# Optimization experiments

Measured on AMD Instinct MI355X. Metric: run time of the kernel, lower is better.

Reference implementation:

```python
import jax, jax.numpy as jnp
import numpy as np

N = 20000      # nodes
E = 320000     # edges
F = 32         # node_feat_dim
H = 128        # hidden_dim
HEADS = 4
DH = 128       # out_channels per head (PyG TransformerConv semantics)
L = 2          # number of GNNBlocks actually built


def _ln(x, s, b, eps=1e-5):
    m = x.mean(-1, keepdims=True)
    v = ((x - m) ** 2).mean(-1, keepdims=True)
    return (x - m) / jnp.sqrt(v + eps) * s + b


def setup_inputs() -> dict:
    key = jax.random.key(0)
    ks = jax.random.split(key, 16)
    nrm = lambda k, sh, sc=0.05: jax.random.normal(k, sh, dtype=jnp.float32) * sc
    inp = {}
    inp['x'] = jax.random.normal(ks[0], (N, F), dtype=jnp.float32)
    inp['edge_index'] = jax.random.randint(ks[1], (2, E), 0, N)
    inp['Win'] = nrm(ks[2], (F, H))
    inp['b_in'] = jnp.zeros((H,), jnp.float32)
    inp['ln1_s'] = jnp.ones((L, H), jnp.float32)
    inp['ln1_b'] = jnp.zeros((L, H), jnp.float32)
    inp['Wq'] = nrm(ks[3], (L, H, HEADS * DH))
    inp['bq'] = jnp.zeros((L, HEADS * DH), jnp.float32)
    inp['Wk'] = nrm(ks[4], (L, H, HEADS * DH))
    inp['bk'] = jnp.zeros((L, HEADS * DH), jnp.float32)
    inp['Wv'] = nrm(ks[5], (L, H, HEADS * DH))
    inp['bv'] = jnp.zeros((L, HEADS * DH), jnp.float32)
    inp['Wskip'] = nrm(ks[6], (L, H, H))
    inp['bskip'] = jnp.zeros((L, H), jnp.float32)
    inp['Wbeta'] = nrm(ks[7], (L, 3 * H, 1))
    inp['ln2_s'] = jnp.ones((L, H), jnp.float32)
    inp['ln2_b'] = jnp.zeros((L, H), jnp.float32)
    inp['W1'] = nrm(ks[8], (L, H, 4 * H))
    inp['b1'] = jnp.zeros((L, 4 * H), jnp.float32)
    inp['W2'] = nrm(ks[9], (L, 4 * H, H))
    inp['b2'] = jnp.zeros((L, H), jnp.float32)
    inp['g1'] = jnp.ones((L,), jnp.float32)
    inp['g2'] = jnp.ones((L,), jnp.float32)
    inp['lno_s'] = jnp.ones((H,), jnp.float32)
    inp['lno_b'] = jnp.zeros((H,), jnp.float32)
    return inp


def reference(x, edge_index, Win, b_in, ln1_s, ln1_b, Wq, bq, Wk, bk, Wv, bv,
              Wskip, bskip, Wbeta, ln2_s, ln2_b, W1, b1, W2, b2, g1, g2,
              lno_s, lno_b):
    src, dst = edge_index[0], edge_index[1]  # messages flow src -> dst
    n = x.shape[0]
    scale = 1.0 / np.sqrt(DH).astype(np.float32)
    h = x @ Win + b_in  # [N,H]
    for l in range(L):
        # --- pre-norm TransformerConv (heads=4, concat=False, beta=True) ---
        hn = _ln(h, ln1_s[l], ln1_b[l])
        q = (hn @ Wq[l] + bq[l]).reshape(n, HEADS, DH)
        k = (hn @ Wk[l] + bk[l]).reshape(n, HEADS, DH)
        v = (hn @ Wv[l] + bv[l]).reshape(n, HEADS, DH)
        # per-edge attention logits [E, HEADS]
        alpha = jnp.einsum('ehd,ehd->eh', q[dst], k[src]) * scale
        # segment softmax over incoming edges of each target node
        amax = jax.ops.segment_max(alpha, dst, num_segments=n)  # [N,HEADS]
        num = jnp.exp(alpha - amax[dst])
        den = jax.ops.segment_sum(num, dst, num_segments=n)      # [N,HEADS]
        a = num / den[dst]                                       # [E,HEADS]
        # scatter-aggregate weighted values, then mean over heads (concat=False)
        agg = jax.ops.segment_sum(a[:, :, None] * v[src], dst, num_segments=n)
        out = agg.mean(axis=1)                                   # [N,H]
        # root skip + beta gate
        xr = hn @ Wskip[l] + bskip[l]
        beta = jax.nn.sigmoid(
            jnp.concatenate([out, xr, out - xr], axis=-1) @ Wbeta[l])  # [N,1]
        attn = beta * xr + (1.0 - beta) * out
        h = h + g1[l] * attn
        # --- pre-norm FFN ---
        hn2 = _ln(h, ln2_s[l], ln2_b[l])
        ffn = jax.nn.gelu(hn2 @ W1[l] + b1[l], approximate=False) @ W2[l] + b2[l]
        h = h + g2[l] * ffn
    return _ln(h, lno_s, lno_b)
```

## Files before the change

kernel.cpp:

```cpp
#include <hip/hip_runtime.h>
#include <hip/hip_bf16.h>
#include <math.h>

#define NN 20000
#define NE 320000

typedef unsigned short ushort_t;
typedef unsigned short ushortx8 __attribute__((ext_vector_type(8)));
typedef short s16x8 __attribute__((ext_vector_type(8)));
typedef float f32x4 __attribute__((ext_vector_type(4)));
typedef float f32x2 __attribute__((ext_vector_type(2)));

__device__ __forceinline__ float us2f(unsigned short u){
  return __uint_as_float(((unsigned)u) << 16);
}
__device__ __forceinline__ unsigned short f2us(float f){
  unsigned u = __float_as_uint(f);
  unsigned r = (u + 0x7fffu + ((u >> 16) & 1u)) >> 16;
  return (unsigned short)r;
}
__device__ __forceinline__ void e4m3x8_to_f32(uint2 d, float* out){
  f32x2 a = __builtin_amdgcn_cvt_pk_f32_fp8(d.x, false);
  f32x2 b = __builtin_amdgcn_cvt_pk_f32_fp8(d.x, true);
  f32x2 c = __builtin_amdgcn_cvt_pk_f32_fp8(d.y, false);
  f32x2 e = __builtin_amdgcn_cvt_pk_f32_fp8(d.y, true);
  out[0] = a.x; out[1] = a.y; out[2] = b.x; out[3] = b.y;
  out[4] = c.x; out[5] = c.y; out[6] = e.x; out[7] = e.y;
}
__device__ __forceinline__ uint2 f32x8_to_e4m3(const float* f){
  unsigned lo = __builtin_amdgcn_cvt_pk_fp8_f32(f[0], f[1], 0u, false);
  lo = __builtin_amdgcn_cvt_pk_fp8_f32(f[2], f[3], lo, true);
  unsigned hi = __builtin_amdgcn_cvt_pk_fp8_f32(f[4], f[5], 0u, false);
  hi = __builtin_amdgcn_cvt_pk_fp8_f32(f[6], f[7], hi, true);
  return make_uint2(lo, hi);
}

__global__ void k_hist(const int* __restrict__ ei, int* __restrict__ deg){
  int e = blockIdx.x * 256 + threadIdx.x;
  if (e < NE) atomicAdd(&deg[ei[NE + e]], 1);
}

__global__ __launch_bounds__(1024) void k_scan(const int* __restrict__ deg,
                                               int* __restrict__ rowst,
                                               int* __restrict__ cur){
  __shared__ int s[1024];
  __shared__ int carry_s;
  int tid = threadIdx.x;
  if (tid == 0) carry_s = 0;
  __syncthreads();
  for (int base = 0; base < NN; base += 1024){
    int v = (base + tid < NN) ? deg[base + tid] : 0;
    s[tid] = v; __syncthreads();
    for (int off = 1; off < 1024; off <<= 1){
      int t = (tid >= off) ? s[tid - off] : 0;
      __syncthreads();
      s[tid] += t;
      __syncthreads();
    }
    int carry = carry_s;
    int excl = carry + s[tid] - v;
    if (base + tid < NN){ rowst[base + tid] = excl; cur[base + tid] = excl; }
    __syncthreads();
    if (tid == 0) carry_s = carry + s[1023];
    __syncthreads();
  }
  if (tid == 0) rowst[NN] = carry_s;
}

__global__ void k_scatter(const int* __restrict__ ei, int* __restrict__ cur,
                          int* __restrict__ srcs){
  int e = blockIdx.x * 256 + threadIdx.x;
  if (e < NE){
    int s = ei[e];
    int d = ei[NE + e];
    int p = atomicAdd(&cur[d], 1);
    srcs[p] = s;
  }
}

__global__ void k_wt(const float* __restrict__ Wq, const float* __restrict__ Wk,
                     const float* __restrict__ Wv, const float* __restrict__ Wsk,
                     const float* __restrict__ W1, const float* __restrict__ W2,
                     const float* __restrict__ bq, const float* __restrict__ bk,
                     const float* __restrict__ bv, const float* __restrict__ bsk,
                     ushort_t* __restrict__ out, float* __restrict__ bcat,
                     int* __restrict__ deg){
  int f = blockIdx.x * 256 + threadIdx.x;
  if (f < 688128){
    float val;
    if (f < 425984){
      int l = f / 212992, idx = f % 212992;
      int n = idx / 128, kk = idx % 128;
      if (n < 512)       val = Wq[(size_t)l * 65536 + kk * 512 + n];
      else if (n < 1024) val = Wk[(size_t)l * 65536 + kk * 512 + (n - 512)];
      else if (n < 1536) val = Wv[(size_t)l * 65536 + kk * 512 + (n - 1024)];
      else               val = Wsk[(size_t)l * 16384 + kk * 128 + (n - 1536)];
    } else if (f < 557056){
      int idx = f - 425984;
      int l = idx / 65536, r = idx % 65536;
      int n = r / 128, kk = r % 128;
      val = W1[(size_t)l * 65536 + kk * 512 + n];
    } else {
      int idx = f - 557056;
      int l = idx / 65536, r = idx % 65536;
      int n = r / 512, kk = r % 512;
      val = W2[(size_t)l * 65536 + kk * 128 + n];
    }
    out[f] = f2us(val);
  } else if (f < 691456){
    int i = f - 688128;
    int l = i / 1664, c = i % 1664;
    float v;
    if (c < 512)       v = bq[l * 512 + c];
    else if (c < 1024) v = bk[l * 512 + c - 512];
    else if (c < 1536) v = bv[l * 512 + c - 1024];
    else               v = bsk[l * 128 + c - 1536];
    bcat[i] = v;
  } else if (f < 711456){
    deg[f - 691456] = 0;
  }
}

__global__ __launch_bounds__(128) void k_inproj(const float* __restrict__ x,
                                                const float* __restrict__ Win,
                                                const float* __restrict__ bin,
                                                float* __restrict__ h){
  __shared__ float sW[32 * 128];
  __shared__ float sx[4][32];
  int tid = threadIdx.x;
  for (int i = 0; i < 32; i++) sW[i * 128 + tid] = Win[i * 128 + tid];
  int r0 = blockIdx.x * 4;
  {
    int r = tid >> 5, kk = tid & 31;
    int gr = r0 + r;
    sx[r][kk] = (gr < NN) ? x[gr * 32 + kk] : 0.f;
  }
  __syncthreads();
  float bias = bin[tid];
  for (int r = 0; r < 4; r++){
    int gr = r0 + r;
    if (gr >= NN) break;
    float acc = bias;
    #pragma unroll
    for (int k2 = 0; k2 < 32; k2++) acc += sx[r][k2] * sW[k2 * 128 + tid];
    h[(size_t)gr * 128 + tid] = acc;
  }
}

template<int OUTBF16>
__global__ void k_ln(const float* __restrict__ in, const float* __restrict__ sc,
                     const float* __restrict__ bi, void* __restrict__ outp, int rows){
  int row = blockIdx.x * 4 + (threadIdx.x >> 6);
  int lane = threadIdx.x & 63;
  if (row >= rows) return;
  const float* p = in + (size_t)row * 128 + lane * 2;
  float x0 = p[0], x1 = p[1];
  float sum = x0 + x1;
  for (int m = 1; m < 64; m <<= 1) sum += __shfl_xor(sum, m);
  float mean = sum * (1.f / 128.f);
  float d0 = x0 - mean, d1 = x1 - mean;
  float vs = d0 * d0 + d1 * d1;
  for (int m = 1; m < 64; m <<= 1) vs += __shfl_xor(vs, m);
  float rstd = rsqrtf(vs * (1.f / 128.f) + 1e-5f);
  int d = lane * 2;
  float o0 = d0 * rstd * sc[d] + bi[d];
  float o1 = d1 * rstd * sc[d + 1] + bi[d + 1];
  if (OUTBF16){
    ushort_t* o = (ushort_t*)outp + (size_t)row * 128 + d;
    o[0] = f2us(o0); o[1] = f2us(o1);
  } else {
    float* o = (float*)outp + (size_t)row * 128 + d;
    o[0] = o0; o[1] = o1;
  }
}

template<int MODE>
__global__ __launch_bounds__(256) void k_mm(const ushort_t* __restrict__ A, int M, int K,
                                            const ushort_t* __restrict__ Bt,
                                            const float* __restrict__ bias,
                                            void* __restrict__ Cp, int ldc,
                                            const float* __restrict__ gptr,
                                            ushort_t* __restrict__ qout,
                                            unsigned char* __restrict__ kvout,
                                            ushort_t* __restrict__ xrout){
  __shared__ ushort_t smem[2 * 128 * 72];
  ushort_t* As = smem;
  ushort_t* Bs = smem + 128 * 72;
  int tid = threadIdx.x;
  int m0 = blockIdx.x * 128, n0 = blockIdx.y * 128;
  int lane = tid & 63, w = tid >> 6;
  int wm = (w >> 1) * 64, wn = (w & 1) * 64;
  int fr = lane & 15, fq = lane >> 4;
  f32x4 acc[4][4];
  #pragma unroll
  for (int i = 0; i < 4; i++)
    #pragma unroll
    for (int j = 0; j < 4; j++) acc[i][j] = (f32x4){0.f, 0.f, 0.f, 0.f};

  for (int k0 = 0; k0 < K; k0 += 64){
    __syncthreads();
    #pragma unroll
    for (int it = 0; it < 4; it++){
      int idx = it * 256 + tid;
      int row = idx >> 3, ks = (idx & 7) * 8;
      int gr = m0 + row; if (gr >= M) gr = M - 1;
      *(ushortx8*)&As[row * 72 + ks] = *(const ushortx8*)(A + (size_t)gr * K + k0 + ks);
      *(ushortx8*)&Bs[row * 72 + ks] = *(const ushortx8*)(Bt + (size_t)(n0 + row) * K + k0 + ks);
    }
    __syncthreads();
    #pragma unroll
    for (int ks = 0; ks < 64; ks += 32){
      s16x8 a[4], b[4];
      #pragma unroll
      for (int i = 0; i < 4; i++)
        a[i] = *(const s16x8*)&As[(wm + i * 16 + fr) * 72 + ks + fq * 8];
      #pragma unroll
      for (int j = 0; j < 4; j++)
        b[j] = *(const s16x8*)&Bs[(wn + j * 16 + fr) * 72 + ks + fq * 8];
      #pragma unroll
      for (int i = 0; i < 4; i++)
        #pragma unroll
        for (int j = 0; j < 4; j++)
          acc[i][j] = __builtin_amdgcn_mfma_f32_16x16x32_bf16(a[i], b[j], acc[i][j], 0, 0, 0);
    }
  }

  if (MODE == 2){
    float g = *gptr;
    #pragma unroll
    for (int i = 0; i < 4; i++){
      int grb = m0 + wm + i * 16 + fq * 4;
      #pragma unroll
      for (int r = 0; r < 4; r++){
        int gr = grb + r;
        if (gr >= M) continue;
        #pragma unroll
        for (int j = 0; j < 4; j++){
          int gc = n0 + wn + j * 16 + fr;
          float c = acc[i][j][r] + bias[gc];
          ((float*)Cp)[(size_t)gr * ldc + gc] += g * c;
        }
      }
    }
    return;
  }

  __syncthreads();
  ushort_t* Cs = smem;
  #pragma unroll
  for (int i = 0; i < 4; i++){
    int rowb = wm + i * 16 + fq * 4;
    #pragma unroll
    for (int j = 0; j < 4; j++){
      int col = wn + j * 16 + fr;
      float bv = bias[n0 + col];
      #pragma unroll
      for (int r = 0; r < 4; r++){
        float c = acc[i][j][r] + bv;
        if (MODE == 1) c = 0.5f * c * (1.f + erff(c * 0.70710678118654752f));
        Cs[(rowb + r) * 136 + col] = f2us(c);
      }
    }
  }
  __syncthreads();
  #pragma unroll
  for (int it = 0; it < 8; it++){
    int idx = it * 256 + tid;
    int row = idx >> 4, seg = idx & 15;
    int gr = m0 + row;
    if (gr >= M) continue;
    ushortx8 cv = *(const ushortx8*)&Cs[row * 136 + seg * 8];
    int gc = n0 + seg * 8;
    if (MODE == 1){
      *(ushortx8*)((ushort_t*)Cp + (size_t)gr * ldc + gc) = cv;
    } else {
      if (n0 < 512){
        *(ushortx8*)(qout + (size_t)gr * 512 + gc) = cv;
      } else if (n0 < 1536){
        float fv[8];
        #pragma unroll
        for (int t = 0; t < 8; t++) fv[t] = us2f(cv[t]);
        *(uint2*)(kvout + (size_t)gr * 1024 + (gc - 512)) = f32x8_to_e4m3(fv);
      } else {
        *(ushortx8*)(xrout + (size_t)gr * 128 + (gc - 1536)) = cv;
      }
    }
  }
}

__global__ void k_alpha(const ushort_t* __restrict__ q, const unsigned char* __restrict__ kv8,
                        const int* __restrict__ rowst, const int* __restrict__ srcs,
                        float* __restrict__ alw){
  int n = blockIdx.x * 4 + (threadIdx.x >> 6);
  int lane = threadIdx.x & 63;
  if (n >= NN) return;
  int s0 = rowst[n], s1 = rowst[n + 1];
  if (s0 == s1) return;
  ushortx8 qv = *((const ushortx8*)(q + (size_t)n * 512) + lane);
  float qf[8];
  #pragma unroll
  for (int t = 0; t < 8; t++) qf[t] = us2f(qv[t]);
  const float scale = 0.08838834764831845f;
  int head = lane >> 4;
  for (int c0 = s0; c0 < s1; c0 += 64){
    int rem = s1 - c0; if (rem > 64) rem = 64;
    int se = (lane < rem) ? srcs[c0 + lane] : 0;
    int j = 0;
    for (; j + 4 <= rem; j += 4){
      int sv[4];
      #pragma unroll
      for (int u = 0; u < 4; u++) sv[u] = __shfl(se, j + u);
      uint2 kd[4];
      #pragma unroll
      for (int u = 0; u < 4; u++)
        kd[u] = *((const uint2*)(kv8 + (size_t)sv[u] * 1024) + lane);
      float p[4] = {0.f, 0.f, 0.f, 0.f};
      #pragma unroll
      for (int u = 0; u < 4; u++){
        float kf[8];
        e4m3x8_to_f32(kd[u], kf);
        #pragma unroll
        for (int t = 0; t < 8; t++) p[u] += qf[t] * kf[t];
      }
      #pragma unroll
      for (int u = 0; u < 4; u++){
        p[u] += __shfl_xor(p[u], 1); p[u] += __shfl_xor(p[u], 2);
        p[u] += __shfl_xor(p[u], 4); p[u] += __shfl_xor(p[u], 8);
      }
      if ((lane & 15) == 0){
        #pragma unroll
        for (int u = 0; u < 4; u++) alw[(size_t)(c0 + j + u) * 4 + head] = __expf(p[u] * scale);
      }
    }
    for (; j < rem; j++){
      int sv0 = __shfl(se, j);
      uint2 kd = *((const uint2*)(kv8 + (size_t)sv0 * 1024) + lane);
      float kf[8];
      e4m3x8_to_f32(kd, kf);
      float p0 = 0.f;
      #pragma unroll
      for (int t = 0; t < 8; t++) p0 += qf[t] * kf[t];
      p0 += __shfl_xor(p0, 1); p0 += __shfl_xor(p0, 2);
      p0 += __shfl_xor(p0, 4); p0 += __shfl_xor(p0, 8);
      if ((lane & 15) == 0) alw[(size_t)(c0 + j) * 4 + head] = __expf(p0 * scale);
    }
  }
}

__global__ void k_node(const float* __restrict__ alw, const unsigned char* __restrict__ kv8,
                       const int* __restrict__ rowst, const int* __restrict__ srcs,
                       const ushort_t* __restrict__ xr, const float* __restrict__ Wb,
                       const float* __restrict__ g1p, float* __restrict__ h,
                       const float* __restrict__ sc2, const float* __restrict__ bi2,
                       ushort_t* __restrict__ hn){
  int n = blockIdx.x * 4 + (threadIdx.x >> 6);
  int lane = threadIdx.x & 63;
  if (n >= NN) return;
  int s0 = rowst[n], s1 = rowst[n + 1];
  int deg = s1 - s0;
  int head = lane >> 4;
  float l = 0.f;
  float acc[8] = {0.f, 0.f, 0.f, 0.f, 0.f, 0.f, 0.f, 0.f};
  for (int c0 = s0; c0 < s1; c0 += 64){
    int rem = s1 - c0; if (rem > 64) rem = 64;
    int se = (lane < rem) ? srcs[c0 + lane] : 0;
    int j = 0;
    for (; j + 4 <= rem; j += 4){
      int sv[4];
      #pragma unroll
      for (int u = 0; u < 4; u++) sv[u] = __shfl(se, j + u);
      uint2 vd[4];
      #pragma unroll
      for (int u = 0; u < 4; u++)
        vd[u] = *((const uint2*)(kv8 + (size_t)sv[u] * 1024 + 512) + lane);
      float wv[4];
      #pragma unroll
      for (int u = 0; u < 4; u++) wv[u] = alw[(size_t)(c0 + j + u) * 4 + head];
      #pragma unroll
      for (int u = 0; u < 4; u++){
        float vf[8];
        e4m3x8_to_f32(vd[u], vf);
        l += wv[u];
        #pragma unroll
        for (int t = 0; t < 8; t++) acc[t] += wv[u] * vf[t];
      }
    }
    for (; j < rem; j++){
      int sv0 = __shfl(se, j);
      uint2 vd = *((const uint2*)(kv8 + (size_t)sv0 * 1024 + 512) + lane);
      float vf[8];
      e4m3x8_to_f32(vd, vf);
      float ww = alw[(size_t)(c0 + j) * 4 + head];
      l += ww;
      #pragma unroll
      for (int t = 0; t < 8; t++) acc[t] += ww * vf[t];
    }
  }
  float inv = deg ? (0.25f / l) : 0.f;
  #pragma unroll
  for (int t = 0; t < 8; t++){
    float r = acc[t] * inv;
    r += __shfl_xor(r, 16); r += __shfl_xor(r, 32);
    acc[t] = r;
  }
  if (lane < 16){
    int d = lane * 8;
    float xv[8];
    {
      ushortx8 xrv = *(const ushortx8*)(xr + (size_t)n * 128 + d);
      #pragma unroll
      for (int t = 0; t < 8; t++) xv[t] = us2f(xrv[t]);
    }
    float pp = 0.f;
    #pragma unroll
    for (int t = 0; t < 8; t++){
      float w0 = Wb[d + t], w1 = Wb[128 + d + t], w2 = Wb[256 + d + t];
      pp += acc[t] * (w0 + w2) + xv[t] * (w1 - w2);
    }
    pp += __shfl_xor(pp, 1); pp += __shfl_xor(pp, 2);
    pp += __shfl_xor(pp, 4); pp += __shfl_xor(pp, 8);
    float beta = 1.f / (1.f + __expf(-pp));
    float g = *g1p;
    float* hp = h + (size_t)n * 128 + d;
    float hv[8];
    {
      float4 h0 = *(const float4*)(hp);
      float4 h1 = *(const float4*)(hp + 4);
      hv[0]=h0.x; hv[1]=h0.y; hv[2]=h0.z; hv[3]=h0.w;
      hv[4]=h1.x; hv[5]=h1.y; hv[6]=h1.z; hv[7]=h1.w;
    }
    #pragma unroll
    for (int t = 0; t < 8; t++)
      hv[t] += g * (beta * xv[t] + (1.f - beta) * acc[t]);
    float s = 0.f;
    #pragma unroll
    for (int t = 0; t < 8; t++) s += hv[t];
    s += __shfl_xor(s, 1); s += __shfl_xor(s, 2);
    s += __shfl_xor(s, 4); s += __shfl_xor(s, 8);
    float mean = s * (1.f / 128.f);
    float vs = 0.f;
    #pragma unroll
    for (int t = 0; t < 8; t++){ float dd = hv[t] - mean; vs += dd * dd; }
    vs += __shfl_xor(vs, 1); vs += __shfl_xor(vs, 2);
    vs += __shfl_xor(vs, 4); vs += __shfl_xor(vs, 8);
    float rstd = rsqrtf(vs * (1.f / 128.f) + 1e-5f);
    *(float4*)(hp) = make_float4(hv[0], hv[1], hv[2], hv[3]);
    *(float4*)(hp + 4) = make_float4(hv[4], hv[5], hv[6], hv[7]);
    ushortx8 hno;
    #pragma unroll
    for (int t = 0; t < 8; t++)
      hno[t] = f2us((hv[t] - mean) * rstd * sc2[d + t] + bi2[d + t]);
    *(ushortx8*)(hn + (size_t)n * 128 + d) = hno;
  }
}

extern "C" void kernel_launch(void* const* d_in, const int* in_sizes, int n_in,
                              void* d_out, int out_size, void* d_ws, size_t ws_size,
                              hipStream_t stream){
  const float* x    = (const float*)d_in[0];
  const int*   ei   = (const int*)d_in[1];
  const float* Win  = (const float*)d_in[2];
  const float* bin  = (const float*)d_in[3];
  const float* ln1s = (const float*)d_in[4];
  const float* ln1b = (const float*)d_in[5];
  const float* Wq   = (const float*)d_in[6];
  const float* bq   = (const float*)d_in[7];
  const float* Wk   = (const float*)d_in[8];
  const float* bk   = (const float*)d_in[9];
  const float* Wv   = (const float*)d_in[10];
  const float* bv   = (const float*)d_in[11];
  const float* Wsk  = (const float*)d_in[12];
  const float* bsk  = (const float*)d_in[13];
  const float* Wbt  = (const float*)d_in[14];
  const float* ln2s = (const float*)d_in[15];
  const float* ln2b = (const float*)d_in[16];
  const float* W1   = (const float*)d_in[17];
  const float* b1   = (const float*)d_in[18];
  const float* W2   = (const float*)d_in[19];
  const float* b2   = (const float*)d_in[20];
  const float* g1   = (const float*)d_in[21];
  const float* g2   = (const float*)d_in[22];
  const float* lnos = (const float*)d_in[23];
  const float* lnob = (const float*)d_in[24];

  char* wsb = (char*)d_ws;
  size_t off = 0;
  float*         h    = (float*)(wsb + off);         off += (size_t)NN * 128 * 4;
  ushort_t*      hn   = (ushort_t*)(wsb + off);      off += (size_t)NN * 128 * 2;
  ushort_t*      qbuf = (ushort_t*)(wsb + off);      off += (size_t)NN * 512 * 2;
  unsigned char* kv8  = (unsigned char*)(wsb + off); off += (size_t)NN * 1024;
  ushort_t*      xrb  = (ushort_t*)(wsb + off);      off += (size_t)NN * 128 * 2;
  ushort_t*      tb   = (ushort_t*)(wsb + off);      off += (size_t)NN * 512 * 2;
  float*         alw  = (float*)(wsb + off);         off += (size_t)NE * 4 * 4;
  ushort_t*      wt   = (ushort_t*)(wsb + off);      off += (size_t)688128 * 2;
  float*         bcat = (float*)(wsb + off);         off += (size_t)3328 * 4;
  int*           deg   = (int*)(wsb + off);          off += (size_t)NN * 4;
  int*           rowst = (int*)(wsb + off);          off += (size_t)(NN + 4) * 4;
  int*           cur   = (int*)(wsb + off);          off += (size_t)NN * 4;
  int*           srcs  = (int*)(wsb + off);          off += (size_t)NE * 4;
  ushort_t* Wcat = wt;
  ushort_t* W1t  = wt + 425984;
  ushort_t* W2t  = wt + 557056;

  k_wt<<<2780, 256, 0, stream>>>(Wq, Wk, Wv, Wsk, W1, W2, bq, bk, bv, bsk, wt, bcat, deg);
  k_hist<<<(NE + 255) / 256, 256, 0, stream>>>(ei, deg);
  k_scan<<<1, 1024, 0, stream>>>(deg, rowst, cur);
  k_scatter<<<(NE + 255) / 256, 256, 0, stream>>>(ei, cur, srcs);
  k_inproj<<<(NN + 3) / 4, 128, 0, stream>>>(x, Win, bin, h);

  dim3 gQ(157, 13), gF1(157, 4), gF2(157, 1);
  for (int l = 0; l < 2; l++){
    k_ln<1><<<(NN + 3) / 4, 256, 0, stream>>>(h, ln1s + l * 128, ln1b + l * 128, hn, NN);
    k_mm<3><<<gQ, 256, 0, stream>>>(hn, NN, 128, Wcat + (size_t)l * 212992, bcat + l * 1664,
                                    nullptr, 0, nullptr, qbuf, kv8, xrb);
    k_alpha<<<(NN + 3) / 4, 256, 0, stream>>>(qbuf, kv8, rowst, srcs, alw);
    k_node<<<(NN + 3) / 4, 256, 0, stream>>>(alw, kv8, rowst, srcs, xrb, Wbt + l * 384,
                                             g1 + l, h, ln2s + l * 128, ln2b + l * 128, hn);
    k_mm<1><<<gF1, 256, 0, stream>>>(hn, NN, 128, W1t + (size_t)l * 65536, b1 + l * 512,
                                     tb, 512, nullptr, nullptr, nullptr, nullptr);
    k_mm<2><<<gF2, 256, 0, stream>>>(tb, NN, 512, W2t + (size_t)l * 65536, b2 + l * 128,
                                     h, 128, g2 + l, nullptr, nullptr, nullptr);
  }
  k_ln<0><<<(NN + 3) / 4, 256, 0, stream>>>(h, lnos, lnob, (float*)d_out, NN);
}
```

Before: 462.5 us.

## Replace shared-memory GEMM with per-wave 64x64 direct-load tiles; unroll edge loops by 8

The GEMM kernel no longer stages A and B tiles through shared memory with block-wide barriers. Each wave now computes its own 64x64 output tile, loading MFMA operands straight from global memory, and uses a private LDS slice only for the output transpose. This removes __syncthreads and staging cost but gives up operand reuse across waves, so global and L2 traffic rises. Separately, the edge loops in the alpha and aggregation kernels are unrolled from 4 to 8 gathers to keep more memory loads in flight.

```diff
diff --git a/kernel.cpp b/kernel.cpp
--- a/kernel.cpp
+++ b/kernel.cpp
@@ -175,21 +175,21 @@
 }
 
 template<int MODE>
-__global__ __launch_bounds__(256) void k_mm(const ushort_t* __restrict__ A, int M, int K,
-                                            const ushort_t* __restrict__ Bt,
-                                            const float* __restrict__ bias,
-                                            void* __restrict__ Cp, int ldc,
-                                            const float* __restrict__ gptr,
-                                            ushort_t* __restrict__ qout,
-                                            unsigned char* __restrict__ kvout,
-                                            ushort_t* __restrict__ xrout){
-  __shared__ ushort_t smem[2 * 128 * 72];
-  ushort_t* As = smem;
-  ushort_t* Bs = smem + 128 * 72;
-  int tid = threadIdx.x;
-  int m0 = blockIdx.x * 128, n0 = blockIdx.y * 128;
-  int lane = tid & 63, w = tid >> 6;
-  int wm = (w >> 1) * 64, wn = (w & 1) * 64;
+__global__ __launch_bounds__(256) void k_mmw(const ushort_t* __restrict__ A, int M, int K,
+                                             const ushort_t* __restrict__ Bt,
+                                             const float* __restrict__ bias,
+                                             void* __restrict__ Cp, int ldc,
+                                             const float* __restrict__ gptr,
+                                             ushort_t* __restrict__ qout,
+                                             unsigned char* __restrict__ kvout,
+                                             ushort_t* __restrict__ xrout,
+                                             int ntiles){
+  __shared__ ushort_t smem[4 * 64 * 68];
+  int tid = threadIdx.x, lane = tid & 63, w = tid >> 6;
+  int gw = blockIdx.x * 4 + w;
+  int mt = gw / ntiles, nt = gw - mt * ntiles;
+  int m0 = mt * 64, n0 = nt * 64;
+  if (m0 >= M) return;
   int fr = lane & 15, fq = lane >> 4;
   f32x4 acc[4][4];
   #pragma unroll
@@ -197,46 +197,38 @@
     #pragma unroll
     for (int j = 0; j < 4; j++) acc[i][j] = (f32x4){0.f, 0.f, 0.f, 0.f};
 
-  for (int k0 = 0; k0 < K; k0 += 64){
-    __syncthreads();
-    #pragma unroll
-    for (int it = 0; it < 4; it++){
-      int idx = it * 256 + tid;
-      int row = idx >> 3, ks = (idx & 7) * 8;
-      int gr = m0 + row; if (gr >= M) gr = M - 1;
-      *(ushortx8*)&As[row * 72 + ks] = *(const ushortx8*)(A + (size_t)gr * K + k0 + ks);
-      *(ushortx8*)&Bs[row * 72 + ks] = *(const ushortx8*)(Bt + (size_t)(n0 + row) * K + k0 + ks);
-    }
-    __syncthreads();
-    #pragma unroll
-    for (int ks = 0; ks < 64; ks += 32){
-      s16x8 a[4], b[4];
-      #pragma unroll
-      for (int i = 0; i < 4; i++)
-        a[i] = *(const s16x8*)&As[(wm + i * 16 + fr) * 72 + ks + fq * 8];
+  const ushort_t* ap[4];
+  const ushort_t* bp[4];
+  #pragma unroll
+  for (int i = 0; i < 4; i++){
+    int r = m0 + i * 16 + fr; if (r >= M) r = M - 1;
+    ap[i] = A + (size_t)r * K + fq * 8;
+    bp[i] = Bt + (size_t)(n0 + i * 16 + fr) * K + fq * 8;
+  }
+  for (int k0 = 0; k0 < K; k0 += 32){
+    s16x8 a[4], b[4];
+    #pragma unroll
+    for (int i = 0; i < 4; i++) a[i] = *(const s16x8*)(ap[i] + k0);
+    #pragma unroll
+    for (int j = 0; j < 4; j++) b[j] = *(const s16x8*)(bp[j] + k0);
+    #pragma unroll
+    for (int i = 0; i < 4; i++)
       #pragma unroll
       for (int j = 0; j < 4; j++)
-        b[j] = *(const s16x8*)&Bs[(wn + j * 16 + fr) * 72 + ks + fq * 8];
-      #pragma unroll
-      for (int i = 0; i < 4; i++)
-        #pragma unroll
-        for (int j = 0; j < 4; j++)
-          acc[i][j] = __builtin_amdgcn_mfma_f32_16x16x32_bf16(a[i], b[j], acc[i][j], 0, 0, 0);
-    }
+        acc[i][j] = __builtin_amdgcn_mfma_f32_16x16x32_bf16(a[i], b[j], acc[i][j], 0, 0, 0);
   }
 
   if (MODE == 2){
     float g = *gptr;
     #pragma unroll
     for (int i = 0; i < 4; i++){
-      int grb = m0 + wm + i * 16 + fq * 4;
       #pragma unroll
       for (int r = 0; r < 4; r++){
-        int gr = grb + r;
+        int gr = m0 + i * 16 + fq * 4 + r;
         if (gr >= M) continue;
         #pragma unroll
         for (int j = 0; j < 4; j++){
-          int gc = n0 + wn + j * 16 + fr;
+          int gc = n0 + j * 16 + fr;
           float c = acc[i][j][r] + bias[gc];
           ((float*)Cp)[(size_t)gr * ldc + gc] += g * c;
         }
@@ -245,31 +237,29 @@
     return;
   }
 
-  __syncthreads();
-  ushort_t* Cs = smem;
+  ushort_t* Cs = smem + w * 64 * 68;
   #pragma unroll
   for (int i = 0; i < 4; i++){
-    int rowb = wm + i * 16 + fq * 4;
+    int rb = i * 16 + fq * 4;
     #pragma unroll
     for (int j = 0; j < 4; j++){
-      int col = wn + j * 16 + fr;
+      int col = j * 16 + fr;
       float bv = bias[n0 + col];
       #pragma unroll
       for (int r = 0; r < 4; r++){
         float c = acc[i][j][r] + bv;
         if (MODE == 1) c = 0.5f * c * (1.f + erff(c * 0.70710678118654752f));
-        Cs[(rowb + r) * 136 + col] = f2us(c);
-      }
-    }
-  }
-  __syncthreads();
+        Cs[(rb + r) * 68 + col] = f2us(c);
+      }
+    }
+  }
+  asm volatile("s_waitcnt lgkmcnt(0)" ::: "memory");
   #pragma unroll
-  for (int it = 0; it < 8; it++){
-    int idx = it * 256 + tid;
-    int row = idx >> 4, seg = idx & 15;
+  for (int pass = 0; pass < 8; pass++){
+    int row = pass * 8 + (lane >> 3), seg = lane & 7;
     int gr = m0 + row;
     if (gr >= M) continue;
-    ushortx8 cv = *(const ushortx8*)&Cs[row * 136 + seg * 8];
+    ushortx8 cv = *(const ushortx8*)&Cs[row * 68 + seg * 8];
     int gc = n0 + seg * 8;
     if (MODE == 1){
       *(ushortx8*)((ushort_t*)Cp + (size_t)gr * ldc + gc) = cv;
@@ -306,30 +296,32 @@
     int rem = s1 - c0; if (rem > 64) rem = 64;
     int se = (lane < rem) ? srcs[c0 + lane] : 0;
     int j = 0;
-    for (; j + 4 <= rem; j += 4){
-      int sv[4];
-      #pragma unroll
-      for (int u = 0; u < 4; u++) sv[u] = __shfl(se, j + u);
-      uint2 kd[4];
-      #pragma unroll
-      for (int u = 0; u < 4; u++)
+    for (; j + 8 <= rem; j += 8){
+      int sv[8];
+      #pragma unroll
+      for (int u = 0; u < 8; u++) sv[u] = __shfl(se, j + u);
+      uint2 kd[8];
+      #pragma unroll
+      for (int u = 0; u < 8; u++)
         kd[u] = *((const uint2*)(kv8 + (size_t)sv[u] * 1024) + lane);
-      float p[4] = {0.f, 0.f, 0.f, 0.f};
-      #pragma unroll
-      for (int u = 0; u < 4; u++){
+      float p[8];
+      #pragma unroll
+      for (int u = 0; u < 8; u++){
         float kf[8];
         e4m3x8_to_f32(kd[u], kf);
+        float s = 0.f;
         #pragma unroll
-        for (int t = 0; t < 8; t++) p[u] += qf[t] * kf[t];
-      }
-      #pragma unroll
-      for (int u = 0; u < 4; u++){
+        for (int t = 0; t < 8; t++) s += qf[t] * kf[t];
+        p[u] = s;
+      }
+      #pragma unroll
+      for (int u = 0; u < 8; u++){
         p[u] += __shfl_xor(p[u], 1); p[u] += __shfl_xor(p[u], 2);
         p[u] += __shfl_xor(p[u], 4); p[u] += __shfl_xor(p[u], 8);
       }
       if ((lane & 15) == 0){
         #pragma unroll
-        for (int u = 0; u < 4; u++) alw[(size_t)(c0 + j + u) * 4 + head] = __expf(p[u] * scale);
+        for (int u = 0; u < 8; u++) alw[(size_t)(c0 + j + u) * 4 + head] = __expf(p[u] * scale);
       }
     }
     for (; j < rem; j++){
@@ -365,19 +357,19 @@
     int rem = s1 - c0; if (rem > 64) rem = 64;
     int se = (lane < rem) ? srcs[c0 + lane] : 0;
     int j = 0;
-    for (; j + 4 <= rem; j += 4){
-      int sv[4];
-      #pragma unroll
-      for (int u = 0; u < 4; u++) sv[u] = __shfl(se, j + u);
-      uint2 vd[4];
-      #pragma unroll
-      for (int u = 0; u < 4; u++)
+    for (; j + 8 <= rem; j += 8){
+      int sv[8];
+      #pragma unroll
+      for (int u = 0; u < 8; u++) sv[u] = __shfl(se, j + u);
+      uint2 vd[8];
+      #pragma unroll
+      for (int u = 0; u < 8; u++)
         vd[u] = *((const uint2*)(kv8 + (size_t)sv[u] * 1024 + 512) + lane);
-      float wv[4];
-      #pragma unroll
-      for (int u = 0; u < 4; u++) wv[u] = alw[(size_t)(c0 + j + u) * 4 + head];
-      #pragma unroll
-      for (int u = 0; u < 4; u++){
+      float wv[8];
+      #pragma unroll
+      for (int u = 0; u < 8; u++) wv[u] = alw[(size_t)(c0 + j + u) * 4 + head];
+      #pragma unroll
+      for (int u = 0; u < 8; u++){
         float vf[8];
         e4m3x8_to_f32(vd[u], vf);
         l += wv[u];
@@ -508,18 +500,20 @@
   k_scatter<<<(NE + 255) / 256, 256, 0, stream>>>(ei, cur, srcs);
   k_inproj<<<(NN + 3) / 4, 128, 0, stream>>>(x, Win, bin, h);
 
-  dim3 gQ(157, 13), gF1(157, 4), gF2(157, 1);
+  int gQKVS = (313 * 26 + 3) / 4;
+  int gFF1  = (313 * 8 + 3) / 4;
+  int gFF2  = (313 * 2 + 3) / 4;
   for (int l = 0; l < 2; l++){
     k_ln<1><<<(NN + 3) / 4, 256, 0, stream>>>(h, ln1s + l * 128, ln1b + l * 128, hn, NN);
-    k_mm<3><<<gQ, 256, 0, stream>>>(hn, NN, 128, Wcat + (size_t)l * 212992, bcat + l * 1664,
-                                    nullptr, 0, nullptr, qbuf, kv8, xrb);
+    k_mmw<3><<<gQKVS, 256, 0, stream>>>(hn, NN, 128, Wcat + (size_t)l * 212992, bcat + l * 1664,
+                                        nullptr, 0, nullptr, qbuf, kv8, xrb, 26);
     k_alpha<<<(NN + 3) / 4, 256, 0, stream>>>(qbuf, kv8, rowst, srcs, alw);
     k_node<<<(NN + 3) / 4, 256, 0, stream>>>(alw, kv8, rowst, srcs, xrb, Wbt + l * 384,
                                              g1 + l, h, ln2s + l * 128, ln2b + l * 128, hn);
-    k_mm<1><<<gF1, 256, 0, stream>>>(hn, NN, 128, W1t + (size_t)l * 65536, b1 + l * 512,
-                                     tb, 512, nullptr, nullptr, nullptr, nullptr);
-    k_mm<2><<<gF2, 256, 0, stream>>>(tb, NN, 512, W2t + (size_t)l * 65536, b2 + l * 128,
-                                     h, 128, g2 + l, nullptr, nullptr, nullptr);
+    k_mmw<1><<<gFF1, 256, 0, stream>>>(hn, NN, 128, W1t + (size_t)l * 65536, b1 + l * 512,
+                                       tb, 512, nullptr, nullptr, nullptr, nullptr, 8);
+    k_mmw<2><<<gFF2, 256, 0, stream>>>(tb, NN, 512, W2t + (size_t)l * 65536, b2 + l * 128,
+                                       h, 128, g2 + l, nullptr, nullptr, nullptr, 2);
   }
   k_ln<0><<<(NN + 3) / 4, 256, 0, stream>>>(h, lnos, lnob, (float*)d_out, NN);
 }
```

New measurement: 494.0 us. 1.07x slower.

## Fuse attention logit pass into aggregation and fold layernorm into FFN2 epilogue

Applied to the files above, without the earlier changes.

Merges the per-edge logit kernel into the node aggregation kernel, so K and V are gathered together and the exp weights are computed on the fly. This removes the edge-weight buffer and its write/read round trip, plus one launch per layer. It also fuses the residual update of the second FFN matmul with the following layernorm (next layer's LN1 or the final output LN) via a shared-memory row tile. The trade-off is higher LDS use in that GEMM, which may lower occupancy, and a serial per-wave LN loop.

```diff
diff --git a/kernel.cpp b/kernel.cpp
--- a/kernel.cpp
+++ b/kernel.cpp
@@ -147,9 +147,8 @@
   }
 }
 
-template<int OUTBF16>
 __global__ void k_ln(const float* __restrict__ in, const float* __restrict__ sc,
-                     const float* __restrict__ bi, void* __restrict__ outp, int rows){
+                     const float* __restrict__ bi, ushort_t* __restrict__ outp, int rows){
   int row = blockIdx.x * 4 + (threadIdx.x >> 6);
   int lane = threadIdx.x & 63;
   if (row >= rows) return;
@@ -163,18 +162,12 @@
   for (int m = 1; m < 64; m <<= 1) vs += __shfl_xor(vs, m);
   float rstd = rsqrtf(vs * (1.f / 128.f) + 1e-5f);
   int d = lane * 2;
-  float o0 = d0 * rstd * sc[d] + bi[d];
-  float o1 = d1 * rstd * sc[d + 1] + bi[d + 1];
-  if (OUTBF16){
-    ushort_t* o = (ushort_t*)outp + (size_t)row * 128 + d;
-    o[0] = f2us(o0); o[1] = f2us(o1);
-  } else {
-    float* o = (float*)outp + (size_t)row * 128 + d;
-    o[0] = o0; o[1] = o1;
-  }
-}
-
-template<int MODE>
+  ushort_t* o = outp + (size_t)row * 128 + d;
+  o[0] = f2us(d0 * rstd * sc[d] + bi[d]);
+  o[1] = f2us(d1 * rstd * sc[d + 1] + bi[d + 1]);
+}
+
+template<int MODE, int LNOUT>
 __global__ __launch_bounds__(256) void k_mm(const ushort_t* __restrict__ A, int M, int K,
                                             const ushort_t* __restrict__ Bt,
                                             const float* __restrict__ bias,
@@ -182,10 +175,14 @@
                                             const float* __restrict__ gptr,
                                             ushort_t* __restrict__ qout,
                                             unsigned char* __restrict__ kvout,
-                                            ushort_t* __restrict__ xrout){
-  __shared__ ushort_t smem[2 * 128 * 72];
-  ushort_t* As = smem;
-  ushort_t* Bs = smem + 128 * 72;
+                                            ushort_t* __restrict__ xrout,
+                                            const float* __restrict__ lnsc,
+                                            const float* __restrict__ lnbi,
+                                            void* __restrict__ lnout){
+  constexpr int SMEM = (MODE == 4) ? (128 * 132 * 4) : (2 * 128 * 72 * 2);
+  __shared__ __align__(16) char smem_raw[SMEM];
+  ushort_t* As = (ushort_t*)smem_raw;
+  ushort_t* Bs = As + 128 * 72;
   int tid = threadIdx.x;
   int m0 = blockIdx.x * 128, n0 = blockIdx.y * 128;
   int lane = tid & 63, w = tid >> 6;
@@ -225,28 +222,56 @@
     }
   }
 
-  if (MODE == 2){
+  if (MODE == 4){
     float g = *gptr;
+    float* fhs = (float*)smem_raw;
+    __syncthreads();
     #pragma unroll
     for (int i = 0; i < 4; i++){
-      int grb = m0 + wm + i * 16 + fq * 4;
       #pragma unroll
       for (int r = 0; r < 4; r++){
-        int gr = grb + r;
+        int lrow = wm + i * 16 + fq * 4 + r;
+        int gr = m0 + lrow;
         if (gr >= M) continue;
         #pragma unroll
         for (int j = 0; j < 4; j++){
-          int gc = n0 + wn + j * 16 + fr;
+          int gc = wn + j * 16 + fr;
           float c = acc[i][j][r] + bias[gc];
-          ((float*)Cp)[(size_t)gr * ldc + gc] += g * c;
+          float hv = ((float*)Cp)[(size_t)gr * 128 + gc] + g * c;
+          ((float*)Cp)[(size_t)gr * 128 + gc] = hv;
+          fhs[lrow * 132 + gc] = hv;
         }
       }
     }
+    __syncthreads();
+    for (int rr = 0; rr < 32; rr++){
+      int lrow = w * 32 + rr;
+      int gr = m0 + lrow;
+      if (gr >= M) break;
+      int d = lane * 2;
+      float x0 = fhs[lrow * 132 + d], x1 = fhs[lrow * 132 + d + 1];
+      float sum = x0 + x1;
+      for (int msk = 1; msk < 64; msk <<= 1) sum += __shfl_xor(sum, msk);
+      float mean = sum * (1.f / 128.f);
+      float d0 = x0 - mean, d1 = x1 - mean;
+      float vs = d0 * d0 + d1 * d1;
+      for (int msk = 1; msk < 64; msk <<= 1) vs += __shfl_xor(vs, msk);
+      float rstd = rsqrtf(vs * (1.f / 128.f) + 1e-5f);
+      float o0 = d0 * rstd * lnsc[d] + lnbi[d];
+      float o1 = d1 * rstd * lnsc[d + 1] + lnbi[d + 1];
+      if (LNOUT){
+        ushort_t* o = (ushort_t*)lnout + (size_t)gr * 128 + d;
+        o[0] = f2us(o0); o[1] = f2us(o1);
+      } else {
+        float* o = (float*)lnout + (size_t)gr * 128 + d;
+        o[0] = o0; o[1] = o1;
+      }
+    }
     return;
   }
 
   __syncthreads();
-  ushort_t* Cs = smem;
+  ushort_t* Cs = (ushort_t*)smem_raw;
   #pragma unroll
   for (int i = 0; i < 4; i++){
     int rowb = wm + i * 16 + fq * 4;
@@ -288,66 +313,7 @@
   }
 }
 
-__global__ void k_alpha(const ushort_t* __restrict__ q, const unsigned char* __restrict__ kv8,
-                        const int* __restrict__ rowst, const int* __restrict__ srcs,
-                        float* __restrict__ alw){
-  int n = blockIdx.x * 4 + (threadIdx.x >> 6);
-  int lane = threadIdx.x & 63;
-  if (n >= NN) return;
-  int s0 = rowst[n], s1 = rowst[n + 1];
-  if (s0 == s1) return;
-  ushortx8 qv = *((const ushortx8*)(q + (size_t)n * 512) + lane);
-  float qf[8];
-  #pragma unroll
-  for (int t = 0; t < 8; t++) qf[t] = us2f(qv[t]);
-  const float scale = 0.08838834764831845f;
-  int head = lane >> 4;
-  for (int c0 = s0; c0 < s1; c0 += 64){
-    int rem = s1 - c0; if (rem > 64) rem = 64;
-    int se = (lane < rem) ? srcs[c0 + lane] : 0;
-    int j = 0;
-    for (; j + 4 <= rem; j += 4){
-      int sv[4];
-      #pragma unroll
-      for (int u = 0; u < 4; u++) sv[u] = __shfl(se, j + u);
-      uint2 kd[4];
-      #pragma unroll
-      for (int u = 0; u < 4; u++)
-        kd[u] = *((const uint2*)(kv8 + (size_t)sv[u] * 1024) + lane);
-      float p[4] = {0.f, 0.f, 0.f, 0.f};
-      #pragma unroll
-      for (int u = 0; u < 4; u++){
-        float kf[8];
-        e4m3x8_to_f32(kd[u], kf);
-        #pragma unroll
-        for (int t = 0; t < 8; t++) p[u] += qf[t] * kf[t];
-      }
-      #pragma unroll
-      for (int u = 0; u < 4; u++){
-        p[u] += __shfl_xor(p[u], 1); p[u] += __shfl_xor(p[u], 2);
-        p[u] += __shfl_xor(p[u], 4); p[u] += __shfl_xor(p[u], 8);
-      }
-      if ((lane & 15) == 0){
-        #pragma unroll
-        for (int u = 0; u < 4; u++) alw[(size_t)(c0 + j + u) * 4 + head] = __expf(p[u] * scale);
-      }
-    }
-    for (; j < rem; j++){
-      int sv0 = __shfl(se, j);
-      uint2 kd = *((const uint2*)(kv8 + (size_t)sv0 * 1024) + lane);
-      float kf[8];
-      e4m3x8_to_f32(kd, kf);
-      float p0 = 0.f;
-      #pragma unroll
-      for (int t = 0; t < 8; t++) p0 += qf[t] * kf[t];
-      p0 += __shfl_xor(p0, 1); p0 += __shfl_xor(p0, 2);
-      p0 += __shfl_xor(p0, 4); p0 += __shfl_xor(p0, 8);
-      if ((lane & 15) == 0) alw[(size_t)(c0 + j) * 4 + head] = __expf(p0 * scale);
-    }
-  }
-}
-
-__global__ void k_node(const float* __restrict__ alw, const unsigned char* __restrict__ kv8,
+__global__ void k_attn(const ushort_t* __restrict__ q, const unsigned char* __restrict__ kv8,
                        const int* __restrict__ rowst, const int* __restrict__ srcs,
                        const ushort_t* __restrict__ xr, const float* __restrict__ Wb,
                        const float* __restrict__ g1p, float* __restrict__ h,
@@ -359,6 +325,11 @@
   int s0 = rowst[n], s1 = rowst[n + 1];
   int deg = s1 - s0;
   int head = lane >> 4;
+  const float scale = 0.08838834764831845f;
+  ushortx8 qv = *((const ushortx8*)(q + (size_t)n * 512) + lane);
+  float qf[8];
+  #pragma unroll
+  for (int t = 0; t < 8; t++) qf[t] = us2f(qv[t]);
   float l = 0.f;
   float acc[8] = {0.f, 0.f, 0.f, 0.f, 0.f, 0.f, 0.f, 0.f};
   for (int c0 = s0; c0 < s1; c0 += 64){
@@ -369,28 +340,53 @@
       int sv[4];
       #pragma unroll
       for (int u = 0; u < 4; u++) sv[u] = __shfl(se, j + u);
-      uint2 vd[4];
-      #pragma unroll
-      for (int u = 0; u < 4; u++)
-        vd[u] = *((const uint2*)(kv8 + (size_t)sv[u] * 1024 + 512) + lane);
-      float wv[4];
-      #pragma unroll
-      for (int u = 0; u < 4; u++) wv[u] = alw[(size_t)(c0 + j + u) * 4 + head];
+      uint2 kd[4], vd[4];
+      #pragma unroll
+      for (int u = 0; u < 4; u++){
+        const unsigned char* base = kv8 + (size_t)sv[u] * 1024;
+        kd[u] = *((const uint2*)(base) + lane);
+        vd[u] = *((const uint2*)(base + 512) + lane);
+      }
+      float p[4];
+      #pragma unroll
+      for (int u = 0; u < 4; u++){
+        float kf[8];
+        e4m3x8_to_f32(kd[u], kf);
+        float s = 0.f;
+        #pragma unroll
+        for (int t = 0; t < 8; t++) s += qf[t] * kf[t];
+        p[u] = s;
+      }
+      #pragma unroll
+      for (int u = 0; u < 4; u++){
+        p[u] += __shfl_xor(p[u], 1); p[u] += __shfl_xor(p[u], 2);
+        p[u] += __shfl_xor(p[u], 4); p[u] += __shfl_xor(p[u], 8);
+      }
       #pragma unroll
       for (int u = 0; u < 4; u++){
         float vf[8];
         e4m3x8_to_f32(vd[u], vf);
-        l += wv[u];
+        float ww = __expf(p[u] * scale);
+        l += ww;
         #pragma unroll
-        for (int t = 0; t < 8; t++) acc[t] += wv[u] * vf[t];
+        for (int t = 0; t < 8; t++) acc[t] += ww * vf[t];
       }
     }
     for (; j < rem; j++){
       int sv0 = __shfl(se, j);
-      uint2 vd = *((const uint2*)(kv8 + (size_t)sv0 * 1024 + 512) + lane);
+      const unsigned char* base = kv8 + (size_t)sv0 * 1024;
+      uint2 kd = *((const uint2*)(base) + lane);
+      uint2 vd = *((const uint2*)(base + 512) + lane);
+      float kf[8];
+      e4m3x8_to_f32(kd, kf);
+      float p0 = 0.f;
+      #pragma unroll
+      for (int t = 0; t < 8; t++) p0 += qf[t] * kf[t];
+      p0 += __shfl_xor(p0, 1); p0 += __shfl_xor(p0, 2);
+      p0 += __shfl_xor(p0, 4); p0 += __shfl_xor(p0, 8);
       float vf[8];
       e4m3x8_to_f32(vd, vf);
-      float ww = alw[(size_t)(c0 + j) * 4 + head];
+      float ww = __expf(p0 * scale);
       l += ww;
       #pragma unroll
       for (int t = 0; t < 8; t++) acc[t] += ww * vf[t];
@@ -491,7 +487,6 @@
   unsigned char* kv8  = (unsigned char*)(wsb + off); off += (size_t)NN * 1024;
   ushort_t*      xrb  = (ushort_t*)(wsb + off);      off += (size_t)NN * 128 * 2;
   ushort_t*      tb   = (ushort_t*)(wsb + off);      off += (size_t)NN * 512 * 2;
-  float*         alw  = (float*)(wsb + off);         off += (size_t)NE * 4 * 4;
   ushort_t*      wt   = (ushort_t*)(wsb + off);      off += (size_t)688128 * 2;
   float*         bcat = (float*)(wsb + off);         off += (size_t)3328 * 4;
   int*           deg   = (int*)(wsb + off);          off += (size_t)NN * 4;
@@ -507,19 +502,26 @@
   k_scan<<<1, 1024, 0, stream>>>(deg, rowst, cur);
   k_scatter<<<(NE + 255) / 256, 256, 0, stream>>>(ei, cur, srcs);
   k_inproj<<<(NN + 3) / 4, 128, 0, stream>>>(x, Win, bin, h);
+  k_ln<<<(NN + 3) / 4, 256, 0, stream>>>(h, ln1s, ln1b, hn, NN);
 
   dim3 gQ(157, 13), gF1(157, 4), gF2(157, 1);
   for (int l = 0; l < 2; l++){
-    k_ln<1><<<(NN + 3) / 4, 256, 0, stream>>>(h, ln1s + l * 128, ln1b + l * 128, hn, NN);
-    k_mm<3><<<gQ, 256, 0, stream>>>(hn, NN, 128, Wcat + (size_t)l * 212992, bcat + l * 1664,
-                                    nullptr, 0, nullptr, qbuf, kv8, xrb);
-    k_alpha<<<(NN + 3) / 4, 256, 0, stream>>>(qbuf, kv8, rowst, srcs, alw);
-    k_node<<<(NN + 3) / 4, 256, 0, stream>>>(alw, kv8, rowst, srcs, xrb, Wbt + l * 384,
+    k_mm<3,0><<<gQ, 256, 0, stream>>>(hn, NN, 128, Wcat + (size_t)l * 212992, bcat + l * 1664,
+                                      nullptr, 0, nullptr, qbuf, kv8, xrb,
+                                      nullptr, nullptr, nullptr);
+    k_attn<<<(NN + 3) / 4, 256, 0, stream>>>(qbuf, kv8, rowst, srcs, xrb, Wbt + l * 384,
                                              g1 + l, h, ln2s + l * 128, ln2b + l * 128, hn);
-    k_mm<1><<<gF1, 256, 0, stream>>>(hn, NN, 128, W1t + (size_t)l * 65536, b1 + l * 512,
-                                     tb, 512, nullptr, nullptr, nullptr, nullptr);
-    k_mm<2><<<gF2, 256, 0, stream>>>(tb, NN, 512, W2t + (size_t)l * 65536, b2 + l * 128,
-                                     h, 128, g2 + l, nullptr, nullptr, nullptr);
-  }
-  k_ln<0><<<(NN + 3) / 4, 256, 0, stream>>>(h, lnos, lnob, (float*)d_out, NN);
-}
+    k_mm<1,0><<<gF1, 256, 0, stream>>>(hn, NN, 128, W1t + (size_t)l * 65536, b1 + l * 512,
+                                       tb, 512, nullptr, nullptr, nullptr, nullptr,
+                                       nullptr, nullptr, nullptr);
+    if (l == 0){
+      k_mm<4,1><<<gF2, 256, 0, stream>>>(tb, NN, 512, W2t, b2, h, 128, g2,
+                                         nullptr, nullptr, nullptr,
+                                         ln1s + 128, ln1b + 128, hn);
+    } else {
+      k_mm<4,0><<<gF2, 256, 0, stream>>>(tb, NN, 512, W2t + 65536, b2 + 128, h, 128, g2 + 1,
+                                         nullptr, nullptr, nullptr,
+                                         lnos, lnob, d_out);
+    }
+  }
+}
```

After: 471.5 us. Within noise of the previous version (+1.9%).
